# Kernel optimization log

Measured on AMD Instinct MI355X. Metric: run time of the kernel, lower is better.

The kernel has to match this reference:

```python
import jax, jax.numpy as jnp
import numpy as np

# Module hyperparameters (init_kwargs): SAN subtraction2 config
K = 7   # kernel_size
S = 1   # stride
P = 3   # padding
D = 1   # dilation
PAD_MODE = 'reflect'  # pad_mode=1 -> reflection padding; pad_mode=0 would be zeros


def _subtraction2(input1, input2):
    """out[n,c,kk,l] = unfold(input2)[n,c,kk,l] - input1[n,c,l].

    input1: [N, C, H_out, W_out] (queries at output locations)
    input2: [N, C, H, W]         (keys, windowed)
    returns [N, C, K*K, H_out*W_out]
    """
    N, C, H, W = input2.shape
    x2 = jnp.pad(input2, ((0, 0), (0, 0), (P, P), (P, P)), mode=PAD_MODE)
    out_h = (H + 2 * P - D * (K - 1) - 1) // S + 1
    out_w = (W + 2 * P - D * (K - 1) - 1) // S + 1
    # Gather the K*K dilated window via shifted strided slices (no im2col buffer
    # beyond the output itself; loop is over the fixed 7x7 kernel footprint).
    patches = []
    for i in range(K):
        for j in range(K):
            patches.append(
                x2[:, :,
                   i * D: i * D + S * (out_h - 1) + 1: S,
                   j * D: j * D + S * (out_w - 1) + 1: S])
    win = jnp.stack(patches, axis=2).reshape(N, C, K * K, out_h * out_w)
    return win - input1.reshape(N, C, 1, out_h * out_w)


def setup_inputs() -> dict:
    key = jax.random.key(0)
    k1, k2 = jax.random.split(key)
    N, C, H, W = 8, 64, 56, 56
    input1 = jax.random.normal(k1, (N, C, H, W), dtype=jnp.float32)
    input2 = jax.random.normal(k2, (N, C, H, W), dtype=jnp.float32)
    return {"input1": input1, "input2": input2}


def reference(input1, input2):
    return _subtraction2(input1, input2)
```

## Files before the change

### kernel.cpp

```cpp
#include <hip/hip_runtime.h>


typedef float f4 __attribute__((ext_vector_type(4)));

#define KSZ 7
#define KK 49
#define HH 56
#define WW 56
#define L 3136
#define W4 14

__device__ __forceinline__ int refl56(int s) {
    s = s < 0 ? -s : s;
    return s >= 56 ? 110 - s : s;
}

__global__ __launch_bounds__(256) void sub2_kernel(
    const float* __restrict__ in1,
    const float* __restrict__ in2,
    float* __restrict__ out)
{
    int i  = blockIdx.x % KSZ;
    int nc = blockIdx.x / KSZ;

    const float* __restrict__ plane1 = in1 + (size_t)nc * L;
    const float* __restrict__ plane2 = in2 + (size_t)nc * L;
    float* __restrict__ outb = out + (size_t)(nc * KK + i * KSZ) * L;

#pragma unroll 1
    for (int t0 = 0; t0 < 784; t0 += 256) {
        int t = t0 + threadIdx.x;
        if (t >= 784) break;

        int oh  = t / W4;
        int ow4 = t % W4;
        int ow  = ow4 * 4;

        const f4 q = *reinterpret_cast<const f4*>(plane1 + oh * WW + ow);

        int rh = refl56(oh + i - 3);
        const float* __restrict__ row = plane2 + rh * WW;

        int b = 4 * ow4 - 4;
        b = b < 0 ? 0 : (b > 44 ? 44 : b);
        const f4 p0 = *reinterpret_cast<const f4*>(row + b);
        const f4 p1 = *reinterpret_cast<const f4*>(row + b + 4);
        const f4 p2 = *reinterpret_cast<const f4*>(row + b + 8);
        float w[12] = {p0.x, p0.y, p0.z, p0.w,
                       p1.x, p1.y, p1.z, p1.w,
                       p2.x, p2.y, p2.z, p2.w};

        bool e0  = (ow4 == 0);
        bool e13 = (ow4 == 13);
        float v[11];
        v[1]  = e0 ? w[3] : (e13 ? w[5]  : w[1]);
        v[2]  = e0 ? w[2] : (e13 ? w[6]  : w[2]);
        v[3]  = e0 ? w[1] : (e13 ? w[7]  : w[3]);
        v[4]  = e0 ? w[0] : (e13 ? w[8]  : w[4]);
        v[5]  = e0 ? w[1] : (e13 ? w[9]  : w[5]);
        v[6]  = e0 ? w[2] : (e13 ? w[10] : w[6]);
        v[7]  = e0 ? w[3] : (e13 ? w[11] : w[7]);
        v[8]  = e0 ? w[4] : (e13 ? w[10] : w[8]);
        v[9]  = e0 ? w[5] : w[9];
        v[10] = e0 ? w[6] : (e13 ? w[8]  : w[10]);

        float* outp = outb + oh * WW + ow;
#pragma unroll
        for (int j = 0; j < KSZ; ++j) {
            f4 r;
            r.x = v[j + 1] - q.x;
            r.y = v[j + 2] - q.y;
            r.z = v[j + 3] - q.z;
            r.w = v[j + 4] - q.w;
            *reinterpret_cast<f4*>(outp) = r;
            outp += L;
        }
    }
}

extern "C" void kernel_launch(void* const* d_in, const int* in_sizes, int n_in,
                              void* d_out, int out_size, void* d_ws, size_t ws_size,
                              hipStream_t stream) {
    const float* in1 = (const float*)d_in[0];
    const float* in2 = (const float*)d_in[1];
    float* out = (float*)d_out;

    int grid = 512 * KSZ;
    sub2_kernel<<<grid, 256, 0, stream>>>(in1, in2, out);
}
```

Measured before the change: 64.01 us.

## Flatten grid to one thread per 4-wide output, loop all kernel rows in-thread

Replaces the per-(plane, kernel-row) block decomposition, which looped over 784 positions with partially idle blocks, with a flat grid where each thread owns one 4-wide output segment. Each thread loads all 7 reflected input rows up front and writes all 49 window offsets. This removes the tail waste of the old loop and issues 21 independent loads at once per thread, at the cost of more registers per thread and larger per-thread store strides across output planes.

```diff
diff --git a/kernel.cpp b/kernel.cpp
--- a/kernel.cpp
+++ b/kernel.cpp
@@ -18,40 +18,44 @@
 __global__ __launch_bounds__(256) void sub2_kernel(
     const float* __restrict__ in1,
     const float* __restrict__ in2,
-    float* __restrict__ out)
+    float* __restrict__ out,
+    int total)
 {
-    int i  = blockIdx.x % KSZ;
-    int nc = blockIdx.x / KSZ;
+    int tid = blockIdx.x * blockDim.x + threadIdx.x;
+    if (tid >= total) return;
 
-    const float* __restrict__ plane1 = in1 + (size_t)nc * L;
+    int t   = tid % 784;
+    int nc  = tid / 784;
+    int oh  = t / W4;
+    int ow4 = t % W4;
+    int ow  = ow4 * 4;
+
     const float* __restrict__ plane2 = in2 + (size_t)nc * L;
-    float* __restrict__ outb = out + (size_t)(nc * KK + i * KSZ) * L;
 
-#pragma unroll 1
-    for (int t0 = 0; t0 < 784; t0 += 256) {
-        int t = t0 + threadIdx.x;
-        if (t >= 784) break;
+    const f4 q = *reinterpret_cast<const f4*>(in1 + (size_t)nc * L + oh * WW + ow);
 
-        int oh  = t / W4;
-        int ow4 = t % W4;
-        int ow  = ow4 * 4;
+    int b = 4 * ow4 - 4;
+    b = b < 0 ? 0 : (b > 44 ? 44 : b);
 
-        const f4 q = *reinterpret_cast<const f4*>(plane1 + oh * WW + ow);
+    f4 p[KSZ][3];
+#pragma unroll
+    for (int i = 0; i < KSZ; ++i) {
+        int rh = refl56(oh + i - 3);
+        const float* __restrict__ row = plane2 + rh * WW + b;
+        p[i][0] = *reinterpret_cast<const f4*>(row);
+        p[i][1] = *reinterpret_cast<const f4*>(row + 4);
+        p[i][2] = *reinterpret_cast<const f4*>(row + 8);
+    }
 
-        int rh = refl56(oh + i - 3);
-        const float* __restrict__ row = plane2 + rh * WW;
+    bool e0  = (ow4 == 0);
+    bool e13 = (ow4 == 13);
+    float* __restrict__ outb = out + ((size_t)nc * KK * L + oh * WW + ow);
 
-        int b = 4 * ow4 - 4;
-        b = b < 0 ? 0 : (b > 44 ? 44 : b);
-        const f4 p0 = *reinterpret_cast<const f4*>(row + b);
-        const f4 p1 = *reinterpret_cast<const f4*>(row + b + 4);
-        const f4 p2 = *reinterpret_cast<const f4*>(row + b + 8);
-        float w[12] = {p0.x, p0.y, p0.z, p0.w,
-                       p1.x, p1.y, p1.z, p1.w,
-                       p2.x, p2.y, p2.z, p2.w};
-
-        bool e0  = (ow4 == 0);
-        bool e13 = (ow4 == 13);
+#pragma unroll
+    for (int i = 0; i < KSZ; ++i) {
+        float w[12] = {p[i][0].x, p[i][0].y, p[i][0].z, p[i][0].w,
+                       p[i][1].x, p[i][1].y, p[i][1].z, p[i][1].w,
+                       p[i][2].x, p[i][2].y, p[i][2].z, p[i][2].w};
         float v[11];
         v[1]  = e0 ? w[3] : (e13 ? w[5]  : w[1]);
         v[2]  = e0 ? w[2] : (e13 ? w[6]  : w[2]);
@@ -64,7 +68,7 @@
         v[9]  = e0 ? w[5] : w[9];
         v[10] = e0 ? w[6] : (e13 ? w[8]  : w[10]);
 
-        float* outp = outb + oh * WW + ow;
+        float* outp = outb + (size_t)i * KSZ * L;
 #pragma unroll
         for (int j = 0; j < KSZ; ++j) {
             f4 r;
@@ -85,6 +89,8 @@
     const float* in2 = (const float*)d_in[1];
     float* out = (float*)d_out;
 
-    int grid = 512 * KSZ;
-    sub2_kernel<<<grid, 256, 0, stream>>>(in1, in2, out);
+    int total = 512 * 784;
+    int block = 256;
+    int grid = (total + block - 1) / block;
+    sub2_kernel<<<grid, block, 0, stream>>>(in1, in2, out, total);
 }
```

New measurement: 63.49 us. About the same (-0.8%).

## Stage input2 plane in LDS and split work per plane into halves

Applied to the files above, without the earlier changes.

Each block now loads the whole 56x56 input2 plane into shared memory once and computes all 7 kernel rows for half of the output positions, instead of one kernel row per block reading from global memory. The aim is to cut repeated global and L2 reads of input2 and in1 (previously re-read by 7 blocks each). The grid shrinks from 3584 to 1024 blocks and each block writes 49 output planes, which changes parallelism and adds a 12.5KB LDS footprint and a barrier. Each thread also has more stores in flight. The kernel is dominated by output writes, so this may not change much.

```diff
diff --git a/kernel.cpp b/kernel.cpp
--- a/kernel.cpp
+++ b/kernel.cpp
@@ -20,60 +20,72 @@
     const float* __restrict__ in2,
     float* __restrict__ out)
 {
-    int i  = blockIdx.x % KSZ;
-    int nc = blockIdx.x / KSZ;
+    __shared__ alignas(16) float lds2[L];
+
+    int half = blockIdx.x & 1;
+    int nc   = blockIdx.x >> 1;
 
     const float* __restrict__ plane1 = in1 + (size_t)nc * L;
     const float* __restrict__ plane2 = in2 + (size_t)nc * L;
-    float* __restrict__ outb = out + (size_t)(nc * KK + i * KSZ) * L;
+    float* __restrict__ outb = out + (size_t)nc * KK * L;
 
+    for (int idx = threadIdx.x; idx < 784; idx += 256) {
+        *reinterpret_cast<f4*>(lds2 + 4 * idx) =
+            *reinterpret_cast<const f4*>(plane2 + 4 * idx);
+    }
+    __syncthreads();
+
+    int t0 = half * 392;
 #pragma unroll 1
-    for (int t0 = 0; t0 < 784; t0 += 256) {
-        int t = t0 + threadIdx.x;
-        if (t >= 784) break;
+    for (int tt = 0; tt < 392; tt += 256) {
+        if (tt + (int)threadIdx.x >= 392) break;
+        int t = t0 + tt + threadIdx.x;
 
         int oh  = t / W4;
         int ow4 = t % W4;
-        int ow  = ow4 * 4;
 
-        const f4 q = *reinterpret_cast<const f4*>(plane1 + oh * WW + ow);
-
-        int rh = refl56(oh + i - 3);
-        const float* __restrict__ row = plane2 + rh * WW;
+        const f4 q = *reinterpret_cast<const f4*>(plane1 + 4 * t);
 
         int b = 4 * ow4 - 4;
         b = b < 0 ? 0 : (b > 44 ? 44 : b);
-        const f4 p0 = *reinterpret_cast<const f4*>(row + b);
-        const f4 p1 = *reinterpret_cast<const f4*>(row + b + 4);
-        const f4 p2 = *reinterpret_cast<const f4*>(row + b + 8);
-        float w[12] = {p0.x, p0.y, p0.z, p0.w,
-                       p1.x, p1.y, p1.z, p1.w,
-                       p2.x, p2.y, p2.z, p2.w};
-
         bool e0  = (ow4 == 0);
         bool e13 = (ow4 == 13);
-        float v[11];
-        v[1]  = e0 ? w[3] : (e13 ? w[5]  : w[1]);
-        v[2]  = e0 ? w[2] : (e13 ? w[6]  : w[2]);
-        v[3]  = e0 ? w[1] : (e13 ? w[7]  : w[3]);
-        v[4]  = e0 ? w[0] : (e13 ? w[8]  : w[4]);
-        v[5]  = e0 ? w[1] : (e13 ? w[9]  : w[5]);
-        v[6]  = e0 ? w[2] : (e13 ? w[10] : w[6]);
-        v[7]  = e0 ? w[3] : (e13 ? w[11] : w[7]);
-        v[8]  = e0 ? w[4] : (e13 ? w[10] : w[8]);
-        v[9]  = e0 ? w[5] : w[9];
-        v[10] = e0 ? w[6] : (e13 ? w[8]  : w[10]);
 
-        float* outp = outb + oh * WW + ow;
+        float* outp0 = outb + 4 * t;
+
 #pragma unroll
-        for (int j = 0; j < KSZ; ++j) {
-            f4 r;
-            r.x = v[j + 1] - q.x;
-            r.y = v[j + 2] - q.y;
-            r.z = v[j + 3] - q.z;
-            r.w = v[j + 4] - q.w;
-            *reinterpret_cast<f4*>(outp) = r;
-            outp += L;
+        for (int i = 0; i < KSZ; ++i) {
+            int rh = refl56(oh + i - 3);
+            const float* __restrict__ row = lds2 + rh * WW + b;
+            const f4 p0 = *reinterpret_cast<const f4*>(row);
+            const f4 p1 = *reinterpret_cast<const f4*>(row + 4);
+            const f4 p2 = *reinterpret_cast<const f4*>(row + 8);
+            float w[12] = {p0.x, p0.y, p0.z, p0.w,
+                           p1.x, p1.y, p1.z, p1.w,
+                           p2.x, p2.y, p2.z, p2.w};
+            float v[11];
+            v[1]  = e0 ? w[3] : (e13 ? w[5]  : w[1]);
+            v[2]  = e0 ? w[2] : (e13 ? w[6]  : w[2]);
+            v[3]  = e0 ? w[1] : (e13 ? w[7]  : w[3]);
+            v[4]  = e0 ? w[0] : (e13 ? w[8]  : w[4]);
+            v[5]  = e0 ? w[1] : (e13 ? w[9]  : w[5]);
+            v[6]  = e0 ? w[2] : (e13 ? w[10] : w[6]);
+            v[7]  = e0 ? w[3] : (e13 ? w[11] : w[7]);
+            v[8]  = e0 ? w[4] : (e13 ? w[10] : w[8]);
+            v[9]  = e0 ? w[5] : w[9];
+            v[10] = e0 ? w[6] : (e13 ? w[8]  : w[10]);
+
+            float* outp = outp0 + (size_t)i * KSZ * L;
+#pragma unroll
+            for (int j = 0; j < KSZ; ++j) {
+                f4 r;
+                r.x = v[j + 1] - q.x;
+                r.y = v[j + 2] - q.y;
+                r.z = v[j + 3] - q.z;
+                r.w = v[j + 4] - q.w;
+                *reinterpret_cast<f4*>(outp) = r;
+                outp += L;
+            }
         }
     }
 }
@@ -85,6 +97,6 @@
     const float* in2 = (const float*)d_in[1];
     float* out = (float*)d_out;
 
-    int grid = 512 * KSZ;
+    int grid = 512 * 2;
     sub2_kernel<<<grid, 256, 0, stream>>>(in1, in2, out);
 }
```

Result: faster. 62.18 us (-2.9%).
